# Kernel optimization log

Hardware: AMD Instinct MI355X
Metric: run time of the kernel (lower is better)

The kernel has to match this reference:

```python
import jax, jax.numpy as jnp
import numpy as np

HIDDEN = 768
NHEADS = 12
HEAD = HIDDEN // NHEADS


def setup_inputs() -> dict:
    key = jax.random.key(0)
    ks = jax.random.split(key, 10)
    B, S = 32, 512
    s = 1.0 / np.sqrt(HIDDEN)
    return {
        "x": jax.random.normal(ks[0], (B, S, HIDDEN), jnp.float32),
        "additive_attention_mask": jnp.zeros((B, 1, 1, S), jnp.float32),
        "Wq": jax.random.normal(ks[1], (HIDDEN, HIDDEN), jnp.float32) * s,
        "bq": jnp.zeros((HIDDEN,), jnp.float32),
        "Wk": jax.random.normal(ks[2], (HIDDEN, HIDDEN), jnp.float32) * s,
        "bk": jnp.zeros((HIDDEN,), jnp.float32),
        "Wv": jax.random.normal(ks[3], (HIDDEN, HIDDEN), jnp.float32) * s,
        "bv": jnp.zeros((HIDDEN,), jnp.float32),
        "Wo": jax.random.normal(ks[4], (HIDDEN, HIDDEN), jnp.float32) * s,
        "bo": jnp.zeros((HIDDEN,), jnp.float32),
    }


def reference(x, additive_attention_mask, Wq, bq, Wk, bk, Wv, bv, Wo, bo):
    B, S, _ = x.shape
    # projections (dropout is identity in eval mode)
    q = (x @ Wq + bq).reshape(B, S, NHEADS, HEAD)
    k = (x @ Wk + bk).reshape(B, S, NHEADS, HEAD)
    v = (x @ Wv + bv).reshape(B, S, NHEADS, HEAD)
    scores = jnp.einsum('bqhd,bkhd->bhqk', q, k) / jnp.sqrt(jnp.float32(HEAD))
    scores = scores + additive_attention_mask  # broadcast [B,1,1,S]
    probs = jax.nn.softmax(scores, axis=-1)
    attn = jnp.einsum('bhqk,bkhd->bqhd', probs, v).reshape(B, S, HIDDEN)
    return attn @ Wo + bo
```

## Files before the change

### kernel.cpp

```cpp
#include <hip/hip_runtime.h>
#include <stdint.h>

typedef unsigned short u16;
typedef __attribute__((ext_vector_type(4))) float floatx4;
typedef __attribute__((ext_vector_type(8))) __bf16 bf16x8;

__device__ __forceinline__ u16 f2bf(float f) {
  uint32_t u = __float_as_uint(f);
  u += 0x7FFFu + ((u >> 16) & 1u);
  return (u16)(u >> 16);
}

__global__ __launch_bounds__(256) void prep_fused_kernel(
    const float* __restrict__ x, u16* __restrict__ xb,
    const float* __restrict__ Wq, const float* __restrict__ Wk,
    const float* __restrict__ Wv, const float* __restrict__ Wo,
    const float* __restrict__ bq, const float* __restrict__ bk, const float* __restrict__ bv,
    u16* __restrict__ Wt, u16* __restrict__ Wto, float* __restrict__ bias) {
  __shared__ u16 sT[64][72];
  const int bx = blockIdx.x;
  const int tid = threadIdx.x;
  if (bx < 6144) {
    int i = bx * 256 + tid;
    const float4* p = (const float4*)x;
    float4 a = p[(size_t)i * 2];
    float4 b = p[(size_t)i * 2 + 1];
    uint32_t w0 = (uint32_t)f2bf(a.x) | ((uint32_t)f2bf(a.y) << 16);
    uint32_t w1 = (uint32_t)f2bf(a.z) | ((uint32_t)f2bf(a.w) << 16);
    uint32_t w2 = (uint32_t)f2bf(b.x) | ((uint32_t)f2bf(b.y) << 16);
    uint32_t w3 = (uint32_t)f2bf(b.z) | ((uint32_t)f2bf(b.w) << 16);
    *(uint4*)(xb + (size_t)i * 8) = make_uint4(w0, w1, w2, w3);
    return;
  }
  const int pid = bx - 6144;
  const int mat = pid / 144;
  const int rem = pid - mat * 144;
  const int ktb = rem % 12, ntb = rem / 12;
  const int kt = ktb * 64, nt = ntb * 64;
  const float* W = mat == 0 ? Wq : mat == 1 ? Wk : mat == 2 ? Wv : Wo;
  const int r = tid >> 2, c4 = tid & 3;
#pragma unroll
  for (int p = 0; p < 4; ++p) {
    int c = c4 * 16 + p * 4;
    float4 v = *(const float4*)&W[(size_t)(kt + r) * 768 + nt + c];
    sT[c + 0][r] = f2bf(v.x);
    sT[c + 1][r] = f2bf(v.y);
    sT[c + 2][r] = f2bf(v.z);
    sT[c + 3][r] = f2bf(v.w);
  }
  __syncthreads();
  const int n = tid >> 2, kq = tid & 3;
  uint4 o0 = *(const uint4*)&sT[n][kq * 16];
  uint4 o1 = *(const uint4*)&sT[n][kq * 16 + 8];
  u16* dst = (mat < 3 ? Wt + ((size_t)(mat * 768 + nt + n)) * 768
                      : Wto + (size_t)(nt + n) * 768) + kt + kq * 16;
  *(uint4*)dst = o0;
  *(uint4*)(dst + 8) = o1;
  if (mat < 3 && ktb == 0 && tid < 64) {
    const float* bs = mat == 0 ? bq : mat == 1 ? bk : bv;
    bias[mat * 768 + nt + tid] = bs[nt + tid];
  }
}

__device__ __forceinline__ void gload16(const void* g, void* l) {
  __builtin_amdgcn_global_load_lds((const __attribute__((address_space(1))) void*)g,
                                   (__attribute__((address_space(3))) void*)l,
                                   16, 0, 0);
}

template <int OUTF32, int SCALEQ>
__global__ __launch_bounds__(256, 4) void gemm_bt_kernel(
    const u16* __restrict__ A, const u16* __restrict__ Bt,
    const float* __restrict__ bias, void* __restrict__ Cv, int ldc) {
  __shared__ __align__(16) u16 Alds[128 * 64];
  __shared__ __align__(16) u16 Blds[128 * 64];
  const int m0 = blockIdx.x * 128, n0 = blockIdx.y * 128;
  const int tid = threadIdx.x;
  const int lane = tid & 63, wid = tid >> 6;
  const int wr = wid >> 1, wc = wid & 1;
  const int l15 = lane & 15, l4 = lane >> 4;
  const int srow = lane >> 3;
  const int csw = (lane & 7) ^ srow;

  floatx4 zz = {0.f, 0.f, 0.f, 0.f};
  floatx4 acc[4][4];
#pragma unroll
  for (int i = 0; i < 4; ++i)
#pragma unroll
    for (int j = 0; j < 4; ++j) acc[i][j] = zz;

  for (int kt = 0; kt < 768; kt += 64) {
#pragma unroll
    for (int i = 0; i < 4; ++i) {
      int u = wid * 4 + i;
      int row = u * 8 + srow;
      gload16(A + (size_t)(m0 + row) * 768 + kt + csw * 8, (char*)Alds + u * 1024);
      gload16(Bt + (size_t)(n0 + row) * 768 + kt + csw * 8, (char*)Blds + u * 1024);
    }
    __syncthreads();
#pragma unroll
    for (int kk = 0; kk < 2; ++kk) {
      bf16x8 af[4], bfr[4];
#pragma unroll
      for (int i = 0; i < 4; ++i) {
        int ra = wr * 64 + i * 16 + l15;
        int rb = wc * 64 + i * 16 + l15;
        af[i]  = *(const bf16x8*)((char*)Alds + ra * 128 + (((kk * 4 + l4) ^ (l15 & 7)) << 4));
        bfr[i] = *(const bf16x8*)((char*)Blds + rb * 128 + (((kk * 4 + l4) ^ (l15 & 7)) << 4));
      }
#pragma unroll
      for (int i = 0; i < 4; ++i)
#pragma unroll
        for (int j = 0; j < 4; ++j)
          acc[i][j] = __builtin_amdgcn_mfma_f32_16x16x32_bf16(af[i], bfr[j], acc[i][j], 0, 0, 0);
    }
    __syncthreads();
  }

  const float qs = (SCALEQ && n0 < 768) ? 0.18033688f : 1.0f;
#pragma unroll
  for (int i = 0; i < 4; ++i) {
    int row = m0 + wr * 64 + i * 16 + l4 * 4;
#pragma unroll
    for (int j = 0; j < 4; ++j) {
      int col = n0 + wc * 64 + j * 16 + l15;
      float bv = bias[col];
#pragma unroll
      for (int r = 0; r < 4; ++r) {
        float v = (acc[i][j][r] + bv) * qs;
        if (OUTF32) ((float*)Cv)[(size_t)(row + r) * ldc + col] = v;
        else        ((u16*)Cv)[(size_t)(row + r) * ldc + col] = f2bf(v);
      }
    }
  }
}

__global__ __launch_bounds__(512, 4) void attn_kernel(const u16* __restrict__ qkv,
                                                      const float* __restrict__ mask,
                                                      u16* __restrict__ ctx) {
  __shared__ __align__(16) char lds[34816];
  char* sK = lds;
  char* sV = lds + 16384;
  float* sM = (float*)(lds + 32768);

  const int bid = blockIdx.x;
  const int wg = (bid & 7) * 192 + (bid >> 3);
  const int qt = wg & 3;
  const int h = (wg >> 2) % 12;
  const int b = wg / 48;

  const int tid = threadIdx.x;
  const int lane = tid & 63, w = tid >> 6;
  const int l15 = lane & 15, l4 = lane >> 4;
  const int hi = lane >> 3, doct = lane & 7;

  const u16* base = qkv + (size_t)b * 512 * 2304 + h * 64;
  const u16* Qg = base;
  const u16* Kg = base + 768;
  const u16* Vg = base + 1536;

  const int csw = doct ^ hi;
  const int vp_ = w * 8 + hi;

  auto stageK = [&](int t) {
    const u16* src = Kg + (size_t)(t * 128 + w * 16) * 2304;
#pragma unroll
    for (int i = 0; i < 2; ++i)
      gload16(src + (size_t)(i * 8 + hi) * 2304 + csw * 8,
              sK + (w * 2 + i) * 1024);
  };
  uint4 vra, vrb;
  auto loadV = [&](int t) {
    const u16* vp = Vg + (size_t)(t * 128 + vp_ * 2) * 2304 + doct * 8;
    vra = *(const uint4*)vp;
    vrb = *(const uint4*)(vp + 2304);
  };
  auto writeV = [&]() {
    const u16* pa = (const u16*)&vra;
    const u16* pb = (const u16*)&vrb;
#pragma unroll
    for (int j = 0; j < 8; ++j) {
      int d = doct * 8 + j;
      uint32_t val = (uint32_t)pa[j] | ((uint32_t)pb[j] << 16);
      *(uint32_t*)(sV + d * 256 +
                   ((4 * vp_) ^ ((d & 7) << 4) ^ (((d >> 3) & 3) << 5))) = val;
    }
  };

  float mval = mask[(size_t)b * 512 + tid];
  stageK(0);
  loadV(0);
  const u16* qp = Qg + (size_t)(qt * 128 + w * 16 + l15) * 2304 + l4 * 8;
  bf16x8 qf0 = *(const bf16x8*)qp;
  bf16x8 qf1 = *(const bf16x8*)(qp + 32);
  sM[tid] = mval * 1.442695f;
  writeV();
  asm volatile("s_waitcnt vmcnt(0) lgkmcnt(0)" ::: "memory");
  __builtin_amdgcn_sched_barrier(0);
  __builtin_amdgcn_s_barrier();

  floatx4 zz = {0.f, 0.f, 0.f, 0.f};
  floatx4 oacc[4];
#pragma unroll
  for (int da = 0; da < 4; ++da) oacc[da] = zz;
  float m_ = -1e30f, l_ = 0.f;

  const int kswz = (l15 & 7) << 4;
  const int src0 = l15 + 32 * (l4 & 1);
  const int src1 = src0 + 16;
  const bool csel = (l4 & 2) != 0;

  for (int t = 0; t < 4; ++t) {
    if (t < 3) loadV(t + 1);

    floatx4 sacc[8];
#pragma unroll
    for (int ct = 0; ct < 8; ++ct) sacc[ct] = zz;
    __builtin_amdgcn_s_setprio(1);
#pragma unroll
    for (int ct = 0; ct < 8; ++ct) {
      const char* kr = sK + (ct * 16 + l15) * 128;
      bf16x8 k0 = *(const bf16x8*)(kr + ((16 * l4) ^ kswz));
      bf16x8 k1 = *(const bf16x8*)(kr + ((64 + 16 * l4) ^ kswz));
      sacc[ct] = __builtin_amdgcn_mfma_f32_16x16x32_bf16(k0, qf0, sacc[ct], 0, 0, 0);
      sacc[ct] = __builtin_amdgcn_mfma_f32_16x16x32_bf16(k1, qf1, sacc[ct], 0, 0, 0);
    }
    __builtin_amdgcn_s_setprio(0);

    float pm = -1e30f;
#pragma unroll
    for (int ct = 0; ct < 8; ++ct) {
      floatx4 mv = *(const floatx4*)(sM + t * 128 + ct * 16 + l4 * 4);
      float v0 = sacc[ct][0] + mv[0];
      float v1 = sacc[ct][1] + mv[1];
      float v2 = sacc[ct][2] + mv[2];
      float v3 = sacc[ct][3] + mv[3];
      sacc[ct][0] = v0; sacc[ct][1] = v1; sacc[ct][2] = v2; sacc[ct][3] = v3;
      pm = fmaxf(pm, fmaxf(fmaxf(v0, v1), fmaxf(v2, v3)));
    }
    pm = fmaxf(pm, __shfl_xor(pm, 16, 64));
    pm = fmaxf(pm, __shfl_xor(pm, 32, 64));
    if (__any(pm > m_ + 11.5416f)) {
      float nm = fmaxf(m_, pm);
      float sc = __builtin_amdgcn_exp2f(m_ - nm);
      m_ = nm;
      l_ *= sc;
#pragma unroll
      for (int da = 0; da < 4; ++da)
#pragma unroll
        for (int j = 0; j < 4; ++j) oacc[da][j] *= sc;
    }
    float ts = 0.f;
#pragma unroll
    for (int ct = 0; ct < 8; ++ct)
#pragma unroll
      for (int j = 0; j < 4; ++j) {
        float e = __builtin_amdgcn_exp2f(sacc[ct][j] - m_);
        sacc[ct][j] = e;
        ts += e;
      }
    ts += __shfl_xor(ts, 16, 64);
    ts += __shfl_xor(ts, 32, 64);
    l_ += ts;

    uint32_t pk[8][2];
#pragma unroll
    for (int ct = 0; ct < 8; ++ct) {
#pragma unroll
      for (int p = 0; p < 2; ++p) {
        uint32_t ua = __float_as_uint(sacc[ct][2 * p]) + 0x8000u;
        uint32_t ub = __float_as_uint(sacc[ct][2 * p + 1]) + 0x8000u;
        pk[ct][p] = (ua >> 16) | (ub & 0xFFFF0000u);
      }
    }

    __builtin_amdgcn_s_setprio(1);
#pragma unroll
    for (int ks = 0; ks < 4; ++ks) {
      uint32_t A0 = __shfl((int)pk[2 * ks][0], src0, 64);
      uint32_t B0 = __shfl((int)pk[2 * ks + 1][0], src0, 64);
      uint32_t A1 = __shfl((int)pk[2 * ks][1], src0, 64);
      uint32_t B1 = __shfl((int)pk[2 * ks + 1][1], src0, 64);
      uint32_t A2 = __shfl((int)pk[2 * ks][0], src1, 64);
      uint32_t B2 = __shfl((int)pk[2 * ks + 1][0], src1, 64);
      uint32_t A3 = __shfl((int)pk[2 * ks][1], src1, 64);
      uint32_t B3 = __shfl((int)pk[2 * ks + 1][1], src1, 64);
      union { uint32_t u[4]; bf16x8 v; } pf;
      pf.u[0] = csel ? B0 : A0;
      pf.u[1] = csel ? B1 : A1;
      pf.u[2] = csel ? B2 : A2;
      pf.u[3] = csel ? B3 : A3;
#pragma unroll
      for (int da = 0; da < 4; ++da) {
        int dd = da * 16 + l15;
        bf16x8 vf = *(const bf16x8*)(sV + dd * 256 +
            ((64 * ks + 16 * l4) ^ ((dd & 7) << 4) ^ (((dd >> 3) & 3) << 5)));
        oacc[da] = __builtin_amdgcn_mfma_f32_16x16x32_bf16(vf, pf.v, oacc[da], 0, 0, 0);
      }
    }
    __builtin_amdgcn_s_setprio(0);

    asm volatile("s_waitcnt lgkmcnt(0)" ::: "memory");
    __builtin_amdgcn_sched_barrier(0);
    __builtin_amdgcn_s_barrier();
    if (t < 3) {
      stageK(t + 1);
      writeV();
      asm volatile("s_waitcnt vmcnt(0) lgkmcnt(0)" ::: "memory");
      __builtin_amdgcn_sched_barrier(0);
      __builtin_amdgcn_s_barrier();
    }
  }

  float rl = 1.0f / l_;
  u16* op = ctx + ((size_t)b * 512 + qt * 128 + w * 16 + l15) * 768 + h * 64;
#pragma unroll
  for (int da = 0; da < 4; ++da) {
    ushort4 o;
    o.x = f2bf(oacc[da][0] * rl);
    o.y = f2bf(oacc[da][1] * rl);
    o.z = f2bf(oacc[da][2] * rl);
    o.w = f2bf(oacc[da][3] * rl);
    *(ushort4*)(op + da * 16 + l4 * 4) = o;
  }
}

extern "C" void kernel_launch(void* const* d_in, const int* in_sizes, int n_in,
                              void* d_out, int out_size, void* d_ws, size_t ws_size,
                              hipStream_t stream) {
  const float* x    = (const float*)d_in[0];
  const float* mask = (const float*)d_in[1];
  const float* Wq   = (const float*)d_in[2];
  const float* bq   = (const float*)d_in[3];
  const float* Wk   = (const float*)d_in[4];
  const float* bk   = (const float*)d_in[5];
  const float* Wv   = (const float*)d_in[6];
  const float* bv   = (const float*)d_in[7];
  const float* Wo   = (const float*)d_in[8];
  const float* bo   = (const float*)d_in[9];
  float* out = (float*)d_out;

  char* ws = (char*)d_ws;
  u16*   xb   = (u16*)ws;
  u16*   ctx  = (u16*)(ws + 25165824);
  u16*   qkv  = (u16*)(ws + 50331648);
  u16*   wtq  = (u16*)(ws + 125829120);
  u16*   wto  = (u16*)(ws + 129368064);
  float* bqkv = (float*)(ws + 130547712);

  prep_fused_kernel<<<6720, 256, 0, stream>>>(x, xb, Wq, Wk, Wv, Wo, bq, bk, bv,
                                              wtq, wto, bqkv);
  gemm_bt_kernel<0, 1><<<dim3(128, 18), 256, 0, stream>>>(xb, wtq, bqkv, (void*)qkv, 2304);
  attn_kernel<<<dim3(1536), dim3(512), 0, stream>>>(qkv, mask, ctx);
  gemm_bt_kernel<1, 0><<<dim3(128, 6), 256, 0, stream>>>(ctx, wto, bo, (void*)out, 768);
}
```

Baseline: 161.2 us.

## Process two query tiles per attention workgroup to reuse staged K/V

Each attention workgroup now handles 256 query rows (two 128-row tiles) instead of 128, so the grid is halved and every K/V tile staged into LDS serves twice as many queries. This removes half of the global K/V loads and LDS staging work. In exchange, each thread holds doubled O accumulators and softmax state, which raises register pressure and may lower occupancy under the 512-thread launch bound. Having fewer workgroups (768) also reduces parallelism across the device.

```diff
diff --git a/kernel.cpp b/kernel.cpp
--- a/kernel.cpp
+++ b/kernel.cpp
@@ -144,10 +144,10 @@
   float* sM = (float*)(lds + 32768);
 
   const int bid = blockIdx.x;
-  const int wg = (bid & 7) * 192 + (bid >> 3);
-  const int qt = wg & 3;
-  const int h = (wg >> 2) % 12;
-  const int b = wg / 48;
+  const int wg = (bid & 7) * 96 + (bid >> 3);
+  const int qh = wg & 1;
+  const int h = (wg >> 1) % 12;
+  const int b = wg / 24;
 
   const int tid = threadIdx.x;
   const int lane = tid & 63, w = tid >> 6;
@@ -190,9 +190,13 @@
   float mval = mask[(size_t)b * 512 + tid];
   stageK(0);
   loadV(0);
-  const u16* qp = Qg + (size_t)(qt * 128 + w * 16 + l15) * 2304 + l4 * 8;
-  bf16x8 qf0 = *(const bf16x8*)qp;
-  bf16x8 qf1 = *(const bf16x8*)(qp + 32);
+  bf16x8 qf0[2], qf1[2];
+#pragma unroll
+  for (int qq = 0; qq < 2; ++qq) {
+    const u16* qp = Qg + (size_t)(qh * 256 + qq * 128 + w * 16 + l15) * 2304 + l4 * 8;
+    qf0[qq] = *(const bf16x8*)qp;
+    qf1[qq] = *(const bf16x8*)(qp + 32);
+  }
   sM[tid] = mval * 1.442695f;
   writeV();
   asm volatile("s_waitcnt vmcnt(0) lgkmcnt(0)" ::: "memory");
@@ -200,10 +204,12 @@
   __builtin_amdgcn_s_barrier();
 
   floatx4 zz = {0.f, 0.f, 0.f, 0.f};
-  floatx4 oacc[4];
-#pragma unroll
-  for (int da = 0; da < 4; ++da) oacc[da] = zz;
-  float m_ = -1e30f, l_ = 0.f;
+  floatx4 oacc[2][4];
+#pragma unroll
+  for (int qq = 0; qq < 2; ++qq)
+#pragma unroll
+    for (int da = 0; da < 4; ++da) oacc[qq][da] = zz;
+  float m_[2] = {-1e30f, -1e30f}, l_[2] = {0.f, 0.f};
 
   const int kswz = (l15 & 7) << 4;
   const int src0 = l15 + 32 * (l4 & 1);
@@ -213,92 +219,95 @@
   for (int t = 0; t < 4; ++t) {
     if (t < 3) loadV(t + 1);
 
-    floatx4 sacc[8];
-#pragma unroll
-    for (int ct = 0; ct < 8; ++ct) sacc[ct] = zz;
-    __builtin_amdgcn_s_setprio(1);
-#pragma unroll
-    for (int ct = 0; ct < 8; ++ct) {
-      const char* kr = sK + (ct * 16 + l15) * 128;
-      bf16x8 k0 = *(const bf16x8*)(kr + ((16 * l4) ^ kswz));
-      bf16x8 k1 = *(const bf16x8*)(kr + ((64 + 16 * l4) ^ kswz));
-      sacc[ct] = __builtin_amdgcn_mfma_f32_16x16x32_bf16(k0, qf0, sacc[ct], 0, 0, 0);
-      sacc[ct] = __builtin_amdgcn_mfma_f32_16x16x32_bf16(k1, qf1, sacc[ct], 0, 0, 0);
-    }
-    __builtin_amdgcn_s_setprio(0);
-
-    float pm = -1e30f;
-#pragma unroll
-    for (int ct = 0; ct < 8; ++ct) {
-      floatx4 mv = *(const floatx4*)(sM + t * 128 + ct * 16 + l4 * 4);
-      float v0 = sacc[ct][0] + mv[0];
-      float v1 = sacc[ct][1] + mv[1];
-      float v2 = sacc[ct][2] + mv[2];
-      float v3 = sacc[ct][3] + mv[3];
-      sacc[ct][0] = v0; sacc[ct][1] = v1; sacc[ct][2] = v2; sacc[ct][3] = v3;
-      pm = fmaxf(pm, fmaxf(fmaxf(v0, v1), fmaxf(v2, v3)));
-    }
-    pm = fmaxf(pm, __shfl_xor(pm, 16, 64));
-    pm = fmaxf(pm, __shfl_xor(pm, 32, 64));
-    if (__any(pm > m_ + 11.5416f)) {
-      float nm = fmaxf(m_, pm);
-      float sc = __builtin_amdgcn_exp2f(m_ - nm);
-      m_ = nm;
-      l_ *= sc;
-#pragma unroll
-      for (int da = 0; da < 4; ++da)
-#pragma unroll
-        for (int j = 0; j < 4; ++j) oacc[da][j] *= sc;
-    }
-    float ts = 0.f;
-#pragma unroll
-    for (int ct = 0; ct < 8; ++ct)
-#pragma unroll
-      for (int j = 0; j < 4; ++j) {
-        float e = __builtin_amdgcn_exp2f(sacc[ct][j] - m_);
-        sacc[ct][j] = e;
-        ts += e;
-      }
-    ts += __shfl_xor(ts, 16, 64);
-    ts += __shfl_xor(ts, 32, 64);
-    l_ += ts;
-
-    uint32_t pk[8][2];
-#pragma unroll
-    for (int ct = 0; ct < 8; ++ct) {
-#pragma unroll
-      for (int p = 0; p < 2; ++p) {
-        uint32_t ua = __float_as_uint(sacc[ct][2 * p]) + 0x8000u;
-        uint32_t ub = __float_as_uint(sacc[ct][2 * p + 1]) + 0x8000u;
-        pk[ct][p] = (ua >> 16) | (ub & 0xFFFF0000u);
-      }
-    }
-
-    __builtin_amdgcn_s_setprio(1);
-#pragma unroll
-    for (int ks = 0; ks < 4; ++ks) {
-      uint32_t A0 = __shfl((int)pk[2 * ks][0], src0, 64);
-      uint32_t B0 = __shfl((int)pk[2 * ks + 1][0], src0, 64);
-      uint32_t A1 = __shfl((int)pk[2 * ks][1], src0, 64);
-      uint32_t B1 = __shfl((int)pk[2 * ks + 1][1], src0, 64);
-      uint32_t A2 = __shfl((int)pk[2 * ks][0], src1, 64);
-      uint32_t B2 = __shfl((int)pk[2 * ks + 1][0], src1, 64);
-      uint32_t A3 = __shfl((int)pk[2 * ks][1], src1, 64);
-      uint32_t B3 = __shfl((int)pk[2 * ks + 1][1], src1, 64);
-      union { uint32_t u[4]; bf16x8 v; } pf;
-      pf.u[0] = csel ? B0 : A0;
-      pf.u[1] = csel ? B1 : A1;
-      pf.u[2] = csel ? B2 : A2;
-      pf.u[3] = csel ? B3 : A3;
-#pragma unroll
-      for (int da = 0; da < 4; ++da) {
-        int dd = da * 16 + l15;
-        bf16x8 vf = *(const bf16x8*)(sV + dd * 256 +
-            ((64 * ks + 16 * l4) ^ ((dd & 7) << 4) ^ (((dd >> 3) & 3) << 5)));
-        oacc[da] = __builtin_amdgcn_mfma_f32_16x16x32_bf16(vf, pf.v, oacc[da], 0, 0, 0);
-      }
-    }
-    __builtin_amdgcn_s_setprio(0);
+#pragma unroll
+    for (int qq = 0; qq < 2; ++qq) {
+      floatx4 sacc[8];
+#pragma unroll
+      for (int ct = 0; ct < 8; ++ct) sacc[ct] = zz;
+      __builtin_amdgcn_s_setprio(1);
+#pragma unroll
+      for (int ct = 0; ct < 8; ++ct) {
+        const char* kr = sK + (ct * 16 + l15) * 128;
+        bf16x8 k0 = *(const bf16x8*)(kr + ((16 * l4) ^ kswz));
+        bf16x8 k1 = *(const bf16x8*)(kr + ((64 + 16 * l4) ^ kswz));
+        sacc[ct] = __builtin_amdgcn_mfma_f32_16x16x32_bf16(k0, qf0[qq], sacc[ct], 0, 0, 0);
+        sacc[ct] = __builtin_amdgcn_mfma_f32_16x16x32_bf16(k1, qf1[qq], sacc[ct], 0, 0, 0);
+      }
+      __builtin_amdgcn_s_setprio(0);
+
+      float pm = -1e30f;
+#pragma unroll
+      for (int ct = 0; ct < 8; ++ct) {
+        floatx4 mv = *(const floatx4*)(sM + t * 128 + ct * 16 + l4 * 4);
+        float v0 = sacc[ct][0] + mv[0];
+        float v1 = sacc[ct][1] + mv[1];
+        float v2 = sacc[ct][2] + mv[2];
+        float v3 = sacc[ct][3] + mv[3];
+        sacc[ct][0] = v0; sacc[ct][1] = v1; sacc[ct][2] = v2; sacc[ct][3] = v3;
+        pm = fmaxf(pm, fmaxf(fmaxf(v0, v1), fmaxf(v2, v3)));
+      }
+      pm = fmaxf(pm, __shfl_xor(pm, 16, 64));
+      pm = fmaxf(pm, __shfl_xor(pm, 32, 64));
+      if (__any(pm > m_[qq] + 11.5416f)) {
+        float nm = fmaxf(m_[qq], pm);
+        float sc = __builtin_amdgcn_exp2f(m_[qq] - nm);
+        m_[qq] = nm;
+        l_[qq] *= sc;
+#pragma unroll
+        for (int da = 0; da < 4; ++da)
+#pragma unroll
+          for (int j = 0; j < 4; ++j) oacc[qq][da][j] *= sc;
+      }
+      float ts = 0.f;
+#pragma unroll
+      for (int ct = 0; ct < 8; ++ct)
+#pragma unroll
+        for (int j = 0; j < 4; ++j) {
+          float e = __builtin_amdgcn_exp2f(sacc[ct][j] - m_[qq]);
+          sacc[ct][j] = e;
+          ts += e;
+        }
+      ts += __shfl_xor(ts, 16, 64);
+      ts += __shfl_xor(ts, 32, 64);
+      l_[qq] += ts;
+
+      uint32_t pk[8][2];
+#pragma unroll
+      for (int ct = 0; ct < 8; ++ct) {
+#pragma unroll
+        for (int p = 0; p < 2; ++p) {
+          uint32_t ua = __float_as_uint(sacc[ct][2 * p]) + 0x8000u;
+          uint32_t ub = __float_as_uint(sacc[ct][2 * p + 1]) + 0x8000u;
+          pk[ct][p] = (ua >> 16) | (ub & 0xFFFF0000u);
+        }
+      }
+
+      __builtin_amdgcn_s_setprio(1);
+#pragma unroll
+      for (int ks = 0; ks < 4; ++ks) {
+        uint32_t A0 = __shfl((int)pk[2 * ks][0], src0, 64);
+        uint32_t B0 = __shfl((int)pk[2 * ks + 1][0], src0, 64);
+        uint32_t A1 = __shfl((int)pk[2 * ks][1], src0, 64);
+        uint32_t B1 = __shfl((int)pk[2 * ks + 1][1], src0, 64);
+        uint32_t A2 = __shfl((int)pk[2 * ks][0], src1, 64);
+        uint32_t B2 = __shfl((int)pk[2 * ks + 1][0], src1, 64);
+        uint32_t A3 = __shfl((int)pk[2 * ks][1], src1, 64);
+        uint32_t B3 = __shfl((int)pk[2 * ks + 1][1], src1, 64);
+        union { uint32_t u[4]; bf16x8 v; } pf;
+        pf.u[0] = csel ? B0 : A0;
+        pf.u[1] = csel ? B1 : A1;
+        pf.u[2] = csel ? B2 : A2;
+        pf.u[3] = csel ? B3 : A3;
+#pragma unroll
+        for (int da = 0; da < 4; ++da) {
+          int dd = da * 16 + l15;
+          bf16x8 vf = *(const bf16x8*)(sV + dd * 256 +
+              ((64 * ks + 16 * l4) ^ ((dd & 7) << 4) ^ (((dd >> 3) & 3) << 5)));
+          oacc[qq][da] = __builtin_amdgcn_mfma_f32_16x16x32_bf16(vf, pf.v, oacc[qq][da], 0, 0, 0);
+        }
+      }
+      __builtin_amdgcn_s_setprio(0);
+    }
 
     asm volatile("s_waitcnt lgkmcnt(0)" ::: "memory");
     __builtin_amdgcn_sched_barrier(0);
@@ -312,16 +321,19 @@
     }
   }
 
-  float rl = 1.0f / l_;
-  u16* op = ctx + ((size_t)b * 512 + qt * 128 + w * 16 + l15) * 768 + h * 64;
-#pragma unroll
-  for (int da = 0; da < 4; ++da) {
-    ushort4 o;
-    o.x = f2bf(oacc[da][0] * rl);
-    o.y = f2bf(oacc[da][1] * rl);
-    o.z = f2bf(oacc[da][2] * rl);
-    o.w = f2bf(oacc[da][3] * rl);
-    *(ushort4*)(op + da * 16 + l4 * 4) = o;
+#pragma unroll
+  for (int qq = 0; qq < 2; ++qq) {
+    float rl = 1.0f / l_[qq];
+    u16* op = ctx + ((size_t)b * 512 + qh * 256 + qq * 128 + w * 16 + l15) * 768 + h * 64;
+#pragma unroll
+    for (int da = 0; da < 4; ++da) {
+      ushort4 o;
+      o.x = f2bf(oacc[qq][da][0] * rl);
+      o.y = f2bf(oacc[qq][da][1] * rl);
+      o.z = f2bf(oacc[qq][da][2] * rl);
+      o.w = f2bf(oacc[qq][da][3] * rl);
+      *(ushort4*)(op + da * 16 + l4 * 4) = o;
+    }
   }
 }
 
@@ -351,6 +363,6 @@
   prep_fused_kernel<<<6720, 256, 0, stream>>>(x, xb, Wq, Wk, Wv, Wo, bq, bk, bv,
                                               wtq, wto, bqkv);
   gemm_bt_kernel<0, 1><<<dim3(128, 18), 256, 0, stream>>>(xb, wtq, bqkv, (void*)qkv, 2304);
-  attn_kernel<<<dim3(1536), dim3(512), 0, stream>>>(qkv, mask, ctx);
+  attn_kernel<<<dim3(768), dim3(512), 0, stream>>>(qkv, mask, ctx);
   gemm_bt_kernel<1, 0><<<dim3(128, 6), 256, 0, stream>>>(ctx, wto, bo, (void*)out, 768);
 }
```

Result: slower. 184.3 us (+14.3%).
